# Optimization experiments

Measured on AMD Instinct MI355X. Metric: run time of the kernel, lower is better.

The kernel has to match this reference:

```python
import jax, jax.numpy as jnp
import numpy as np

N, E, D, H, ED = 10000, 160000, 512, 256, 16
EPS = 1e-5  # BatchNorm1d eps


def _cgconv(x, src, dst, edge_attr, Wf, bf, Ws, bs, gamma, beta, mean, var):
    # PyG CGConv: z = [x_i, x_j, e_ij]; m = sigmoid(lin_f(z)) * softplus(lin_s(z));
    # aggr='add' at target i; batch_norm (eval mode, running stats) then residual.
    z = jnp.concatenate([x[dst], x[src], edge_attr], axis=1)  # [E, 2D+ED]
    m = jax.nn.sigmoid(z @ Wf + bf) * jax.nn.softplus(z @ Ws + bs)  # [E, D]
    aggr = jax.ops.segment_sum(m, dst, num_segments=x.shape[0])  # [N, D]
    bn = (aggr - mean) * jax.lax.rsqrt(var + EPS) * gamma + beta
    return x + bn


def _gcnconv(x, src, dst, W, b):
    # PyG GCNConv with add_self_loops=True, normalize=True:
    n = x.shape[0]
    deg = jax.ops.segment_sum(jnp.ones((src.shape[0],), x.dtype), dst, num_segments=n) + 1.0
    dinv = jax.lax.rsqrt(deg)  # [N]
    h = x @ W  # [N, out]
    out = jax.ops.segment_sum((dinv[src] * dinv[dst])[:, None] * h[src], dst, num_segments=n)
    out = out + (dinv * dinv)[:, None] * h  # self-loop contribution
    return out + b


def _forward(x, edge_attr, goal_feat,
             cg1_Wf, cg1_bf, cg1_Ws, cg1_bs, cg1_gamma, cg1_beta, cg1_mean, cg1_var,
             cg2_Wf, cg2_bf, cg2_Ws, cg2_bs, cg2_gamma, cg2_beta, cg2_mean, cg2_var,
             gcn3_W, gcn3_b, gcn4_W, gcn4_b, d1_W, d1_b, d2_W, d2_b, src, dst):
    # dropout layers are identity in eval mode (self.training=False)
    x = jax.nn.relu(_cgconv(x, src, dst, edge_attr, cg1_Wf, cg1_bf, cg1_Ws, cg1_bs,
                            cg1_gamma, cg1_beta, cg1_mean, cg1_var))
    x = jax.nn.relu(_cgconv(x, src, dst, edge_attr, cg2_Wf, cg2_bf, cg2_Ws, cg2_bs,
                            cg2_gamma, cg2_beta, cg2_mean, cg2_var))
    x = jax.nn.relu(_gcnconv(x, src, dst, gcn3_W, gcn3_b))
    x = jax.nn.relu(_gcnconv(x, src, dst, gcn4_W, gcn4_b))
    g = jnp.broadcast_to(goal_feat, (x.shape[0], goal_feat.shape[1]))  # repeat(num_nodes, 1)
    h = jax.nn.relu(jnp.concatenate([x, g], axis=1) @ d1_W + d1_b)
    return h @ d2_W + d2_b  # [N, 1]


def setup_inputs() -> dict:
    ks = jax.random.split(jax.random.key(0), 12)
    w = lambda k, s: jax.random.normal(k, s, dtype=jnp.float32) * 0.02
    Z = 2 * D + ED
    return {
        "x": jax.random.normal(ks[0], (N, D), jnp.float32),
        "edge_attr": jax.random.normal(ks[1], (E, ED), jnp.float32),
        "goal_feat": jax.random.normal(ks[2], (1, D), jnp.float32),
        "cg1_Wf": w(ks[3], (Z, D)), "cg1_bf": jnp.zeros((D,), jnp.float32),
        "cg1_Ws": w(ks[4], (Z, D)), "cg1_bs": jnp.zeros((D,), jnp.float32),
        "cg1_gamma": jnp.ones((D,), jnp.float32), "cg1_beta": jnp.zeros((D,), jnp.float32),
        "cg1_mean": jnp.zeros((D,), jnp.float32), "cg1_var": jnp.ones((D,), jnp.float32),
        "cg2_Wf": w(ks[5], (Z, D)), "cg2_bf": jnp.zeros((D,), jnp.float32),
        "cg2_Ws": w(ks[6], (Z, D)), "cg2_bs": jnp.zeros((D,), jnp.float32),
        "cg2_gamma": jnp.ones((D,), jnp.float32), "cg2_beta": jnp.zeros((D,), jnp.float32),
        "cg2_mean": jnp.zeros((D,), jnp.float32), "cg2_var": jnp.ones((D,), jnp.float32),
        "gcn3_W": w(ks[7], (D, H)), "gcn3_b": jnp.zeros((H,), jnp.float32),
        "gcn4_W": w(ks[8], (H, H)), "gcn4_b": jnp.zeros((H,), jnp.float32),
        "d1_W": w(ks[9], (H + D, D)), "d1_b": jnp.zeros((D,), jnp.float32),
        "d2_W": w(ks[10], (D, 1)), "d2_b": jnp.zeros((1,), jnp.float32),
        "edge_index": jax.random.randint(ks[11], (2, E), 0, N, dtype=jnp.int32),
        "batch": jnp.zeros((N,), jnp.int32),
    }


def reference(x, edge_attr, goal_feat,
              cg1_Wf, cg1_bf, cg1_Ws, cg1_bs, cg1_gamma, cg1_beta, cg1_mean, cg1_var,
              cg2_Wf, cg2_bf, cg2_Ws, cg2_bs, cg2_gamma, cg2_beta, cg2_mean, cg2_var,
              gcn3_W, gcn3_b, gcn4_W, gcn4_b, d1_W, d1_b, d2_W, d2_b,
              edge_index, batch):
    src, dst = edge_index[0], edge_index[1]
    return _forward(x, edge_attr, goal_feat,
                    cg1_Wf, cg1_bf, cg1_Ws, cg1_bs, cg1_gamma, cg1_beta, cg1_mean, cg1_var,
                    cg2_Wf, cg2_bf, cg2_Ws, cg2_bs, cg2_gamma, cg2_beta, cg2_mean, cg2_var,
                    gcn3_W, gcn3_b, gcn4_W, gcn4_b, d1_W, d1_b, d2_W, d2_b, src, dst)
```

## Files before the change

### kernel.cpp

```cpp
#include <hip/hip_runtime.h>
#include <math.h>

#define N_NODES 10000
#define N_EDGES 160000
#define DIM 512
#define HDIM 256
#define EDIM 16
#define BN_EPS 1e-5f
#define L2E 1.4426950408889634f
#define LN2 0.6931471805599453f

typedef unsigned short ushort_t;
typedef unsigned int uint_t;
typedef __attribute__((ext_vector_type(8))) short bf16x8;
typedef __attribute__((ext_vector_type(4))) float f32x4;
typedef __attribute__((ext_vector_type(2))) _Float16 half2_t;

__device__ __forceinline__ ushort_t f2bf(float x) {
    uint_t u = __float_as_uint(x);
    uint_t r = (u + 0x7FFF + ((u >> 16) & 1)) >> 16;
    return (ushort_t)r;
}
__device__ __forceinline__ float bf2f(ushort_t h) {
    return __uint_as_float(((uint_t)h) << 16);
}
__device__ __forceinline__ float bflo(uint_t u) {
    return __uint_as_float(u << 16);
}
__device__ __forceinline__ float bfhi(uint_t u) {
    return __uint_as_float(u & 0xffff0000u);
}
__device__ __forceinline__ uint_t pk_bf(float a, float b) {
    return (uint_t)f2bf(a) | ((uint_t)f2bf(b) << 16);
}
__device__ __forceinline__ half2_t u2h(uint_t u) {
    return __builtin_bit_cast(half2_t, u);
}
__device__ __forceinline__ uint_t pk_f16(float a, float b) {
    return __builtin_bit_cast(uint_t, __builtin_amdgcn_cvt_pkrtz(a, b));
}
__device__ __forceinline__ void gld16(const void* g, void* l) {
    __builtin_amdgcn_global_load_lds(
        (const __attribute__((address_space(1))) unsigned int*)g,
        (__attribute__((address_space(3))) unsigned int*)l, 16, 0, 0);
}
__device__ __forceinline__ float fexp2(float x) {
#if __has_builtin(__builtin_amdgcn_exp2f)
    return __builtin_amdgcn_exp2f(x);
#else
    return __expf(x * LN2);
#endif
}
__device__ __forceinline__ float flog2(float x) {
#if __has_builtin(__builtin_amdgcn_logf)
    return __builtin_amdgcn_logf(x);
#else
    return __logf(x) * L2E;
#endif
}
__device__ __forceinline__ void swz(int lid, int gx, int gy, int& bx, int& by) {
    int per = gy * 8;
    int grp = lid / per;
    int rem = lid - grp * per;
    int gsz = min(8, gx - grp * 8);
    by = rem / gsz;
    bx = grp * 8 + (rem - by * gsz);
}

__global__ void k_hist(const int* __restrict__ dst, int* __restrict__ cnt) {
    int e = blockIdx.x * blockDim.x + threadIdx.x;
    if (e < N_EDGES) atomicAdd(&cnt[dst[e]], 1);
}

__global__ __launch_bounds__(1024) void k_scan(int* __restrict__ offs, float* __restrict__ dinv) {
    __shared__ int wsum[16];
    __shared__ int carryS;
    int t = threadIdx.x, lane = t & 63, wv = t >> 6;
    if (t == 0) carryS = 0;
    __syncthreads();
    for (int base = 0; base < N_NODES; base += 1024) {
        int idx = base + t;
        int v = (idx < N_NODES) ? offs[idx] : 0;
        if (idx < N_NODES) dinv[idx] = rsqrtf((float)v + 1.0f);
        int s = v;
#pragma unroll
        for (int off = 1; off < 64; off <<= 1) {
            int u = __shfl_up(s, off, 64);
            if (lane >= off) s += u;
        }
        if (lane == 63) wsum[wv] = s;
        __syncthreads();
        int carry = carryS;
        if (wv == 0) {
            int w = (lane < 16) ? wsum[lane] : 0;
#pragma unroll
            for (int off = 1; off < 16; off <<= 1) {
                int u = __shfl_up(w, off, 64);
                if (lane >= off) w += u;
            }
            if (lane < 16) wsum[lane] = w;
        }
        __syncthreads();
        int wbase = (wv == 0) ? 0 : wsum[wv - 1];
        if (idx < N_NODES) offs[idx] = carry + wbase + s - v;
        int total = wsum[15];
        __syncthreads();
        if (t == 0) carryS = carry + total;
        __syncthreads();
    }
    if (t == 0) offs[N_NODES] = carryS;
}

__global__ void k_scatter(const int* __restrict__ srcv, const int* __restrict__ dstv,
                          const float* __restrict__ ea,
                          const int* __restrict__ offs, const float* __restrict__ dinv,
                          int* __restrict__ cursor,
                          int* __restrict__ srcArr, float* __restrict__ dinvArr,
                          uint_t* __restrict__ eaP) {
    int e = blockIdx.x * blockDim.x + threadIdx.x;
    if (e >= N_EDGES) return;
    int d = dstv[e];
    int p = offs[d] + atomicAdd(&cursor[d], 1);
    int s = srcv[e];
    srcArr[p] = s;
    dinvArr[p] = dinv[s];
    const float* er = ea + (size_t)e * EDIM;
    uint_t pk[8];
#pragma unroll
    for (int k2 = 0; k2 < 8; k2++) pk[k2] = pk_f16(er[2 * k2], er[2 * k2 + 1]);
    uint_t* q = eaP + (size_t)p * 8;
    *(uint4*)q = *(uint4*)&pk[0];
    *(uint4*)(q + 4) = *(uint4*)&pk[4];
}

__global__ __launch_bounds__(256) void k_cvtW(
    const float* __restrict__ Wf0, const float* __restrict__ Ws0,
    const float* __restrict__ Wf1, const float* __restrict__ Ws1,
    const float* __restrict__ g3W, const float* __restrict__ g4W,
    const float* __restrict__ d1W,
    ushort_t* __restrict__ W2cg0, ushort_t* __restrict__ W2cg1,
    ushort_t* __restrict__ W2g3, ushort_t* __restrict__ W2g4,
    ushort_t* __restrict__ W2d1,
    int* __restrict__ offsZ, int* __restrict__ curZ, float* __restrict__ outZ)
{
    __shared__ ushort_t tle[64][72];
    int b = blockIdx.x, t = threadIdx.x;
    if (b >= 592) {
        int idx = (b - 592) * 256 + t;
        if (idx < 10001) offsZ[idx] = 0;
        else if (idx < 20001) curZ[idx - 10001] = 0;
        else if (idx < 30001) outZ[idx - 20001] = 0.f;
        return;
    }
    const float* src; int ldw, kin0, cin0, ldk, cout0, kout0; ushort_t* out; float scale;
    if (b < 512) {
        int layer = b >> 8, tt = b & 255;
        int g = tt >> 6, rem = tt & 63;
        int ct = rem >> 3, kt = rem & 7;
        const float* Wf = layer ? Wf1 : Wf0;
        const float* Ws = layer ? Ws1 : Ws0;
        src = (g & 1) ? Ws : Wf;
        ldw = 512; kin0 = ((g & 2) ? 512 : 0) + kt * 64; cin0 = ct * 64;
        out = layer ? W2cg1 : W2cg0; ldk = 512;
        cout0 = g * 512 + ct * 64; kout0 = kt * 64;
        scale = L2E;
    } else if (b < 544) {
        int tt = b - 512; int ct = tt >> 3, kt = tt & 7;
        src = g3W; ldw = 256; kin0 = kt * 64; cin0 = ct * 64;
        out = W2g3; ldk = 512; cout0 = ct * 64; kout0 = kt * 64; scale = 1.f;
    } else if (b < 560) {
        int tt = b - 544; int ct = tt >> 2, kt = tt & 3;
        src = g4W; ldw = 256; kin0 = kt * 64; cin0 = ct * 64;
        out = W2g4; ldk = 256; cout0 = ct * 64; kout0 = kt * 64; scale = 1.f;
    } else {
        int tt = b - 560; int ct = tt >> 2, kt = tt & 3;
        src = d1W; ldw = 512; kin0 = kt * 64; cin0 = ct * 64;
        out = W2d1; ldk = 256; cout0 = ct * 64; kout0 = kt * 64; scale = 1.f;
    }
    int c = t & 63;
    int k4 = t >> 6;
#pragma unroll
    for (int i = 0; i < 16; i++) {
        int k = k4 * 16 + i;
        tle[k][c] = f2bf(src[(size_t)(kin0 + k) * ldw + cin0 + c] * scale);
    }
    __syncthreads();
    int cl = t >> 2, kq = t & 3;
    ushort_t tmp[16];
#pragma unroll
    for (int j = 0; j < 16; j++) tmp[j] = tle[kq * 16 + j][cl];
    ushort_t* dst = out + (size_t)(cout0 + cl) * ldk + kout0 + kq * 16;
    *(uint4*)dst = *(uint4*)&tmp[0];
    *(uint4*)(dst + 8) = *(uint4*)&tmp[8];
}

#define MP_WEP   32
#define MP_GV    40
#define MP_END   20040

__global__ __launch_bounds__(256) void k_megaprep(
    const float* __restrict__ x, const float* __restrict__ goal,
    const float* __restrict__ Wf0, const float* __restrict__ Ws0,
    const float* __restrict__ Wf1, const float* __restrict__ Ws1,
    const float* __restrict__ d1W, const float* __restrict__ d1b,
    ushort_t* __restrict__ A2, uint_t* __restrict__ WEP, float* __restrict__ cgv)
{
    int b = blockIdx.x, t = threadIdx.x;
    if (b < MP_WEP) {
        int layer = b >> 4, blk = b & 15;
        int idx = blk * 256 + t;
        int c = idx >> 3, k2 = idx & 7;
        const float* Wf = (layer ? Wf1 : Wf0) + 1024 * 512;
        const float* Ws = (layer ? Ws1 : Ws0) + 1024 * 512;
        uint_t* WEPf = WEP + layer * 8192;
        uint_t* WEPs = WEPf + 4096;
        WEPf[c * 8 + k2] = pk_f16(Wf[(2 * k2) * 512 + c] * L2E, Wf[(2 * k2 + 1) * 512 + c] * L2E);
        WEPs[c * 8 + k2] = pk_f16(Ws[(2 * k2) * 512 + c] * L2E, Ws[(2 * k2 + 1) * 512 + c] * L2E);
    } else if (b < MP_GV) {
        __shared__ float red[256];
        int bb = b - MP_WEP;
        int c = bb * 64 + (t & 63);
        int slice = t >> 6;
        float acc = 0.f;
        for (int i = 0; i < 128; i++) {
            int k = slice * 128 + i;
            acc += goal[k] * d1W[(size_t)(256 + k) * 512 + c];
        }
        red[t] = acc;
        __syncthreads();
        if (t < 128) red[t] += red[t + 128];
        __syncthreads();
        if (t < 64) cgv[c] = red[t] + red[t + 64] + d1b[c];
    } else {
        int idx = (b - MP_GV) * 256 + t;
        if (idx < N_NODES * 512) A2[idx] = f2bf(x[idx]);
    }
}

__global__ __launch_bounds__(256) void k_gemm3(
    const ushort_t* __restrict__ A2, int K, int M,
    const ushort_t* __restrict__ W2t,
    float* __restrict__ outF, ushort_t* __restrict__ outQ,
    const float* __restrict__ bias, int mode, int ldc, int gx, int gy)
{
    __shared__ ushort_t As[128 * 64];
    __shared__ ushort_t Bs[128 * 64];
    int tid = threadIdx.x;
    int lane = tid & 63, w = tid >> 6;
    int wm = w & 1, wn = w >> 1;
    int lrow = lane & 15, quad = lane >> 4;
    int bx, by;
    swz(blockIdx.x, gx, gy, bx, by);
    int row0 = bx * 128, col0 = by * 128;

    f32x4 acc[4][4] = {};

    const ushort_t* ArG[4]; ushort_t* ArL[4];
    const ushort_t* BrG[4]; ushort_t* BrL[4];
#pragma unroll
    for (int p = 0; p < 4; p++) {
        int s = tid + 256 * p;
        int r = s >> 3, k8p = s & 7;
        int k8l = k8p ^ (r & 7);
        int gra = row0 + r; if (gra >= M) gra = M - 1;
        ArG[p] = A2 + (size_t)gra * K + k8l * 8;
        ArL[p] = As + s * 8;
        BrG[p] = W2t + (size_t)(col0 + r) * K + k8l * 8;
        BrL[p] = Bs + s * 8;
    }
    const ushort_t* afp[2][4];
    const ushort_t* bfp[2][4];
#pragma unroll
    for (int sl = 0; sl < 2; sl++)
#pragma unroll
        for (int mt = 0; mt < 4; mt++) {
            int r = wm * 64 + mt * 16 + lrow;
            afp[sl][mt] = As + (r * 8 + ((sl * 4 + quad) ^ (r & 7))) * 8;
            int c = wn * 64 + mt * 16 + lrow;
            bfp[sl][mt] = Bs + (c * 8 + ((sl * 4 + quad) ^ (c & 7))) * 8;
        }

    for (int k0 = 0; k0 < K; k0 += 64) {
        __syncthreads();
#pragma unroll
        for (int p = 0; p < 4; p++) {
            gld16(ArG[p] + k0, ArL[p]);
            gld16(BrG[p] + k0, BrL[p]);
        }
        __syncthreads();
#pragma unroll
        for (int sl = 0; sl < 2; sl++) {
            bf16x8 af[4], bff[4];
#pragma unroll
            for (int i = 0; i < 4; i++) {
                af[i]  = *(const bf16x8*)afp[sl][i];
                bff[i] = *(const bf16x8*)bfp[sl][i];
            }
#pragma unroll
            for (int mt = 0; mt < 4; mt++)
#pragma unroll
                for (int nt = 0; nt < 4; nt++)
                    acc[mt][nt] = __builtin_amdgcn_mfma_f32_16x16x32_bf16(
                        af[mt], bff[nt], acc[mt][nt], 0, 0, 0);
        }
    }

#pragma unroll
    for (int mt = 0; mt < 4; mt++) {
#pragma unroll
        for (int nt = 0; nt < 4; nt++) {
            int gcol = col0 + wn * 64 + nt * 16 + lrow;
#pragma unroll
            for (int r = 0; r < 4; r++) {
                int grow = row0 + wm * 64 + mt * 16 + quad * 4 + r;
                if (grow >= M) continue;
                float v = acc[mt][nt][r];
                if (mode == 1) {
                    if (gcol < 1024) {
                        outF[(size_t)grow * 1024 + gcol] = v;
                    } else {
                        int c = gcol - 1024;
                        int grp = c >> 9, cc = c & 511;
                        int pos = (cc >> 1) * 4 + grp * 2 + (cc & 1);
                        outQ[(size_t)grow * 1024 + pos] = f2bf(v);
                    }
                } else if (mode == 2) {
                    outF[(size_t)grow * ldc + gcol] = fmaxf(v + bias[gcol], 0.f);
                } else {
                    outQ[(size_t)grow * ldc + gcol] = f2bf(v);
                }
            }
        }
    }
}

__global__ __launch_bounds__(256) void k_gemm64(
    const ushort_t* __restrict__ A2, int K, int M,
    const ushort_t* __restrict__ W2t,
    float* __restrict__ outF, ushort_t* __restrict__ outQ,
    const float* __restrict__ bias, int mode, int ldc, int gx, int gy,
    const float* __restrict__ d2w, const float* __restrict__ d2b,
    float* __restrict__ outG)
{
    __shared__ ushort_t As[64 * 64];
    __shared__ ushort_t Bs[128 * 64];
    __shared__ float part[64];
    int tid = threadIdx.x;
    int lane = tid & 63, w = tid >> 6;
    int lrow = lane & 15, quad = lane >> 4;
    int bx, by;
    swz(blockIdx.x, gx, gy, bx, by);
    int row0 = bx * 64, col0 = by * 128;

    f32x4 acc[4][2] = {};

    const ushort_t* ArG[2]; ushort_t* ArL[2];
    const ushort_t* BrG[4]; ushort_t* BrL[4];
#pragma unroll
    for (int p = 0; p < 2; p++) {
        int s = tid + 256 * p;
        int r = s >> 3, k8p = s & 7;
        int k8l = k8p ^ (r & 7);
        int gra = row0 + r; if (gra >= M) gra = M - 1;
        ArG[p] = A2 + (size_t)gra * K + k8l * 8;
        ArL[p] = As + s * 8;
    }
#pragma unroll
    for (int p = 0; p < 4; p++) {
        int s = tid + 256 * p;
        int r = s >> 3, k8p = s & 7;
        int k8l = k8p ^ (r & 7);
        BrG[p] = W2t + (size_t)(col0 + r) * K + k8l * 8;
        BrL[p] = Bs + s * 8;
    }
    const ushort_t* afp[2][4];
    const ushort_t* bfp[2][2];
#pragma unroll
    for (int sl = 0; sl < 2; sl++) {
#pragma unroll
        for (int mt = 0; mt < 4; mt++) {
            int r = mt * 16 + lrow;
            afp[sl][mt] = As + (r * 8 + ((sl * 4 + quad) ^ (r & 7))) * 8;
        }
#pragma unroll
        for (int nt = 0; nt < 2; nt++) {
            int c = w * 32 + nt * 16 + lrow;
            bfp[sl][nt] = Bs + (c * 8 + ((sl * 4 + quad) ^ (c & 7))) * 8;
        }
    }

    if (mode == 4 && tid < 64) part[tid] = 0.f;

    for (int k0 = 0; k0 < K; k0 += 64) {
        __syncthreads();
        gld16(ArG[0] + k0, ArL[0]);
        gld16(ArG[1] + k0, ArL[1]);
#pragma unroll
        for (int p = 0; p < 4; p++) gld16(BrG[p] + k0, BrL[p]);
        __syncthreads();
#pragma unroll
        for (int sl = 0; sl < 2; sl++) {
            bf16x8 af[4], bff[2];
#pragma unroll
            for (int i = 0; i < 4; i++) af[i] = *(const bf16x8*)afp[sl][i];
#pragma unroll
            for (int i = 0; i < 2; i++) bff[i] = *(const bf16x8*)bfp[sl][i];
#pragma unroll
            for (int mt = 0; mt < 4; mt++)
#pragma unroll
                for (int nt = 0; nt < 2; nt++)
                    acc[mt][nt] = __builtin_amdgcn_mfma_f32_16x16x32_bf16(
                        af[mt], bff[nt], acc[mt][nt], 0, 0, 0);
        }
    }

    if (mode == 4) {
        float w2c[2], bc[2];
#pragma unroll
        for (int nt = 0; nt < 2; nt++) {
            int gcol = col0 + w * 32 + nt * 16 + lrow;
            w2c[nt] = d2w[gcol];
            bc[nt] = bias[gcol];
        }
        __syncthreads();
#pragma unroll
        for (int mt = 0; mt < 4; mt++) {
#pragma unroll
            for (int r = 0; r < 4; r++) {
                float rp = 0.f;
#pragma unroll
                for (int nt = 0; nt < 2; nt++) {
                    float v = fmaxf(acc[mt][nt][r] + bc[nt], 0.f);
                    rp = fmaf(v, w2c[nt], rp);
                }
                atomicAdd(&part[mt * 16 + quad * 4 + r], rp);
            }
        }
        __syncthreads();
        if (tid < 64) {
            int grow = row0 + tid;
            if (grow < M) {
                float v = part[tid];
                if (by == 0) v += d2b[0];
                atomicAdd(&outG[grow], v);
            }
        }
        return;
    }

#pragma unroll
    for (int mt = 0; mt < 4; mt++) {
#pragma unroll
        for (int nt = 0; nt < 2; nt++) {
            int gcol = col0 + w * 32 + nt * 16 + lrow;
#pragma unroll
            for (int r = 0; r < 4; r++) {
                int grow = row0 + mt * 16 + quad * 4 + r;
                if (grow >= M) continue;
                float v = acc[mt][nt][r];
                if (mode == 2) outF[(size_t)grow * ldc + gcol] = fmaxf(v + bias[gcol], 0.f);
                else outQ[(size_t)grow * ldc + gcol] = f2bf(v);
            }
        }
    }
}

__global__ __launch_bounds__(256) void k_cg_aggr(
    const float* __restrict__ xin, const float* __restrict__ P,
    const ushort_t* __restrict__ Qi,
    const uint_t* __restrict__ WEPf, const uint_t* __restrict__ WEPs,
    const float* __restrict__ bfv, const float* __restrict__ bsv,
    const float* __restrict__ gamma, const float* __restrict__ beta,
    const float* __restrict__ mean, const float* __restrict__ var,
    const int* __restrict__ offs, const int* __restrict__ srcArr,
    const uint_t* __restrict__ eaP,
    float* __restrict__ xout, ushort_t* __restrict__ A2out)
{
    int i = blockIdx.x;
    int t = threadIdx.x;
    int c0 = 2 * t;
    uint_t wfp[2][8], wsp[2][8];
    {
        const uint_t* pf8 = WEPf + c0 * 8;
        const uint_t* ps8 = WEPs + c0 * 8;
        *(uint4*)&wfp[0][0] = *(const uint4*)(pf8 + 0);
        *(uint4*)&wfp[0][4] = *(const uint4*)(pf8 + 4);
        *(uint4*)&wfp[1][0] = *(const uint4*)(pf8 + 8);
        *(uint4*)&wfp[1][4] = *(const uint4*)(pf8 + 12);
        *(uint4*)&wsp[0][0] = *(const uint4*)(ps8 + 0);
        *(uint4*)&wsp[0][4] = *(const uint4*)(ps8 + 4);
        *(uint4*)&wsp[1][0] = *(const uint4*)(ps8 + 8);
        *(uint4*)&wsp[1][4] = *(const uint4*)(ps8 + 12);
    }
    float2 pf = *(const float2*)&P[(size_t)i * 1024 + c0];
    float2 ps = *(const float2*)&P[(size_t)i * 1024 + 512 + c0];
    float2 bf2 = *(const float2*)&bfv[c0];
    float2 bs2 = *(const float2*)&bsv[c0];
    pf.x = fmaf(bf2.x, L2E, pf.x); pf.y = fmaf(bf2.y, L2E, pf.y);
    ps.x = fmaf(bs2.x, L2E, ps.x); ps.y = fmaf(bs2.y, L2E, ps.y);
    float acc0 = 0.f, acc1 = 0.f;
    int e0 = offs[i], e1 = offs[i + 1];
    __shared__ uint_t sEaP[32][8];
    __shared__ int sSrc[34];
    const ushort_t* Qbase = Qi + 4 * t;
    for (int base = e0; base < e1; base += 32) {
        int g = min(32, e1 - base);
        __syncthreads();
        if (t < 34) {
            int s = 0;
            if (t < g) s = srcArr[base + t];
            sSrc[t] = s;
        }
        {
            int j = t >> 3, k2 = t & 7;
            if (j < g) sEaP[j][k2] = eaP[(size_t)(base + j) * 8 + k2];
        }
        __syncthreads();
        uint2 q0 = *(const uint2*)(Qbase + ((size_t)sSrc[0] << 10));
        uint2 q1 = *(const uint2*)(Qbase + ((size_t)sSrc[1] << 10));
        for (int j = 0; j < g; j++) {
            uint2 qn = *(const uint2*)(Qbase + ((size_t)sSrc[j + 2] << 10));
            uint4 eA = *(const uint4*)&sEaP[j][0];
            uint4 eB = *(const uint4*)&sEaP[j][4];
            float gf0 = pf.x + bflo(q0.x), gf1 = pf.y + bfhi(q0.x);
            float gs0 = ps.x + bflo(q0.y), gs1 = ps.y + bfhi(q0.y);
            uint_t ek[8] = {eA.x, eA.y, eA.z, eA.w, eB.x, eB.y, eB.z, eB.w};
#pragma unroll
            for (int k = 0; k < 8; k++) {
                half2_t e2 = u2h(ek[k]);
                gf0 = __builtin_amdgcn_fdot2(e2, u2h(wfp[0][k]), gf0, false);
                gf1 = __builtin_amdgcn_fdot2(e2, u2h(wfp[1][k]), gf1, false);
                gs0 = __builtin_amdgcn_fdot2(e2, u2h(wsp[0][k]), gs0, false);
                gs1 = __builtin_amdgcn_fdot2(e2, u2h(wsp[1][k]), gs1, false);
            }
            float sg0 = __builtin_amdgcn_rcpf(1.f + fexp2(-gf0));
            float sg1 = __builtin_amdgcn_rcpf(1.f + fexp2(-gf1));
            float sp0 = fmaxf(gs0, 0.f) + flog2(1.f + fexp2(-fabsf(gs0)));
            float sp1 = fmaxf(gs1, 0.f) + flog2(1.f + fexp2(-fabsf(gs1)));
            acc0 = fmaf(sg0, sp0, acc0);
            acc1 = fmaf(sg1, sp1, acc1);
            q0 = q1; q1 = qn;
        }
    }
    acc0 *= LN2;
    acc1 *= LN2;
    size_t ib = (size_t)i * DIM;
    float2 mn = *(const float2*)&mean[c0];
    float2 vr = *(const float2*)&var[c0];
    float2 gm = *(const float2*)&gamma[c0];
    float2 bt = *(const float2*)&beta[c0];
    float2 xi = *(const float2*)&xin[ib + c0];
    float bn0 = (acc0 - mn.x) * rsqrtf(vr.x + BN_EPS) * gm.x + bt.x;
    float bn1 = (acc1 - mn.y) * rsqrtf(vr.y + BN_EPS) * gm.y + bt.y;
    float o0 = fmaxf(xi.x + bn0, 0.f);
    float o1 = fmaxf(xi.y + bn1, 0.f);
    if (xout) *(float2*)&xout[ib + c0] = make_float2(o0, o1);
    *(uint_t*)(A2out + (size_t)i * 512 + c0) = pk_bf(o0, o1);
}

__global__ __launch_bounds__(128) void k_gcn_aggr(
    const ushort_t* __restrict__ h, const float* __restrict__ dinv,
    const float* __restrict__ bias,
    const int* __restrict__ offs, const int* __restrict__ srcArr,
    const float* __restrict__ dinvArr, ushort_t* __restrict__ A2out)
{
    int i = blockIdx.x;
    int t = threadIdx.x;
    int c0 = 2 * t;
    float acc0 = 0.f, acc1 = 0.f;
    int e0 = offs[i], e1 = offs[i + 1];
    __shared__ int sS[36];
    __shared__ float sD[36];
    for (int base = e0; base < e1; base += 32) {
        int g = min(32, e1 - base);
        __syncthreads();
        if (t < 36) {
            bool ok = (t < g);
            sS[t] = ok ? srcArr[base + t] : 0;
            sD[t] = ok ? dinvArr[base + t] : 0.f;
        }
        __syncthreads();
        uint_t q0 = *(const uint_t*)(h + (size_t)sS[0] * HDIM + c0);
        uint_t q1 = *(const uint_t*)(h + (size_t)sS[1] * HDIM + c0);
        uint_t q2 = *(const uint_t*)(h + (size_t)sS[2] * HDIM + c0);
        uint_t q3 = *(const uint_t*)(h + (size_t)sS[3] * HDIM + c0);
        for (int j = 0; j < g; j++) {
            uint_t qn = *(const uint_t*)(h + (size_t)sS[j + 4] * HDIM + c0);
            acc0 += sD[j] * bflo(q0);
            acc1 += sD[j] * bfhi(q0);
            q0 = q1; q1 = q2; q2 = q3; q3 = qn;
        }
    }
    float di = dinv[i];
    uint_t qi = *(const uint_t*)(h + (size_t)i * HDIM + c0);
    float2 b2 = *(const float2*)&bias[c0];
    float o0 = fmaxf(di * acc0 + di * di * bflo(qi) + b2.x, 0.f);
    float o1 = fmaxf(di * acc1 + di * di * bfhi(qi) + b2.y, 0.f);
    *(uint_t*)(A2out + (size_t)i * 256 + c0) = pk_bf(o0, o1);
}

extern "C" void kernel_launch(void* const* d_in, const int* in_sizes, int n_in,
                              void* d_out, int out_size, void* d_ws, size_t ws_size,
                              hipStream_t stream) {
    (void)in_sizes; (void)n_in; (void)out_size; (void)ws_size;
    const float* x      = (const float*)d_in[0];
    const float* ea     = (const float*)d_in[1];
    const float* goal   = (const float*)d_in[2];
    const float* cgWf[2] = {(const float*)d_in[3],  (const float*)d_in[11]};
    const float* cgbf[2] = {(const float*)d_in[4],  (const float*)d_in[12]};
    const float* cgWs[2] = {(const float*)d_in[5],  (const float*)d_in[13]};
    const float* cgbs[2] = {(const float*)d_in[6],  (const float*)d_in[14]};
    const float* cggm[2] = {(const float*)d_in[7],  (const float*)d_in[15]};
    const float* cgbt[2] = {(const float*)d_in[8],  (const float*)d_in[16]};
    const float* cgmn[2] = {(const float*)d_in[9],  (const float*)d_in[17]};
    const float* cgvr[2] = {(const float*)d_in[10], (const float*)d_in[18]};
    const float* gcn3_W = (const float*)d_in[19];
    const float* gcn3_b = (const float*)d_in[20];
    const float* gcn4_W = (const float*)d_in[21];
    const float* gcn4_b = (const float*)d_in[22];
    const float* d1_W   = (const float*)d_in[23];
    const float* d1_b   = (const float*)d_in[24];
    const float* d2_W   = (const float*)d_in[25];
    const float* d2_b   = (const float*)d_in[26];
    const int*   eidx   = (const int*)d_in[27];
    const int*   srcv   = eidx;
    const int*   dstv   = eidx + N_EDGES;
    float* outp = (float*)d_out;

    char* w = (char*)d_ws;
    float*    Pbuf  = (float*)w;                      w += (size_t)N_NODES * 1024 * 4;
    ushort_t* Qbuf  = (ushort_t*)w;                   w += (size_t)N_NODES * 1024 * 2;
    float*    xB    = (float*)w;                      w += (size_t)N_NODES * 512 * 4;
    ushort_t* A2    = (ushort_t*)w;                   w += (size_t)N_NODES * 512 * 2;
    ushort_t* A3    = (ushort_t*)w;                   w += (size_t)N_NODES * 256 * 2;
    ushort_t* W2cg0 = (ushort_t*)w;                   w += (size_t)2048 * 512 * 2;
    ushort_t* W2cg1 = (ushort_t*)w;                   w += (size_t)2048 * 512 * 2;
    ushort_t* W2g3  = (ushort_t*)w;                   w += (size_t)256 * 512 * 2;
    ushort_t* W2g4  = (ushort_t*)w;                   w += (size_t)256 * 256 * 2;
    ushort_t* W2d1  = (ushort_t*)w;                   w += (size_t)512 * 256 * 2;
    uint_t*   eaP   = (uint_t*)w;                     w += (size_t)N_EDGES * 8 * 4;
    uint_t*   WEP   = (uint_t*)w;                     w += 16384 * 4;
    float*    cgv   = (float*)w;                      w += 512 * 4;
    int*      srcArr  = (int*)w;                      w += N_EDGES * 4;
    float*    dinvArr = (float*)w;                    w += N_EDGES * 4;
    int*      offs    = (int*)w;                      w += (N_NODES + 1) * 4;
    int*      cursor  = (int*)w;                      w += N_NODES * 4;
    float*    dinv    = (float*)w;                    w += N_NODES * 4;
    uint_t* WEPf[2] = {WEP, WEP + 8192};
    uint_t* WEPs[2] = {WEP + 4096, WEP + 12288};
    ushort_t* h3 = (ushort_t*)Pbuf;

    k_cvtW<<<710, 256, 0, stream>>>(cgWf[0], cgWs[0], cgWf[1], cgWs[1],
                                    gcn3_W, gcn4_W, d1_W,
                                    W2cg0, W2cg1, W2g3, W2g4, W2d1,
                                    offs, cursor, outp);
    k_megaprep<<<MP_END, 256, 0, stream>>>(x, goal,
        cgWf[0], cgWs[0], cgWf[1], cgWs[1], d1_W, d1_b, A2, WEP, cgv);

    k_hist<<<(N_EDGES + 255) / 256, 256, 0, stream>>>(dstv, offs);
    k_scan<<<1, 1024, 0, stream>>>(offs, dinv);
    k_scatter<<<(N_EDGES + 255) / 256, 256, 0, stream>>>(srcv, dstv, ea, offs, dinv,
                                                         cursor, srcArr, dinvArr, eaP);

    k_gemm3<<<79 * 16, 256, 0, stream>>>(A2, 512, N_NODES, W2cg0,
                                         Pbuf, Qbuf, nullptr, 1, 0, 79, 16);
    k_cg_aggr<<<N_NODES, 256, 0, stream>>>(x, Pbuf, Qbuf, WEPf[0], WEPs[0],
                                           cgbf[0], cgbs[0],
                                           cggm[0], cgbt[0], cgmn[0], cgvr[0],
                                           offs, srcArr, eaP, xB, A2);
    k_gemm3<<<79 * 16, 256, 0, stream>>>(A2, 512, N_NODES, W2cg1,
                                         Pbuf, Qbuf, nullptr, 1, 0, 79, 16);
    k_cg_aggr<<<N_NODES, 256, 0, stream>>>(xB, Pbuf, Qbuf, WEPf[1], WEPs[1],
                                           cgbf[1], cgbs[1],
                                           cggm[1], cgbt[1], cgmn[1], cgvr[1],
                                           offs, srcArr, eaP, nullptr, A2);

    k_gemm64<<<157 * 2, 256, 0, stream>>>(A2, 512, N_NODES, W2g3,
                                          nullptr, h3, nullptr, 3, HDIM, 157, 2,
                                          nullptr, nullptr, nullptr);
    k_gcn_aggr<<<N_NODES, 128, 0, stream>>>(h3, dinv, gcn3_b, offs, srcArr, dinvArr, A3);

    k_gemm64<<<157 * 2, 256, 0, stream>>>(A3, 256, N_NODES, W2g4,
                                          nullptr, h3, nullptr, 3, HDIM, 157, 2,
                                          nullptr, nullptr, nullptr);
    k_gcn_aggr<<<N_NODES, 128, 0, stream>>>(h3, dinv, gcn4_b, offs, srcArr, dinvArr, A3);

    k_gemm64<<<157 * 4, 256, 0, stream>>>(A3, 256, N_NODES, W2d1,
                                          nullptr, nullptr, cgv, 4, DIM, 157, 4,
                                          d2_W, d2_b, outp);
}
```

Baseline: 563.1 us.

## Compute edge-attribute projection with bf16 MFMA per 8-edge chunk in CG aggregation

Replaces the per-thread fp16 dot2 loop that projected the 16-dim edge attributes onto each channel with a per-chunk bf16 MFMA. It computes the projections for 8 edges across all 512 channels into shared memory, and the per-edge loop then reads them back. Edge attributes and edge weights are now packed as bf16 rather than fp16, which lowers precision. Chunks shrink from 32 to 8 edges, so there are more barriers, half of each 16-row MFMA is wasted, and the weights are reloaded from global memory for every chunk.

```diff
diff --git a/kernel.cpp b/kernel.cpp
--- a/kernel.cpp
+++ b/kernel.cpp
@@ -14,7 +14,6 @@
 typedef unsigned int uint_t;
 typedef __attribute__((ext_vector_type(8))) short bf16x8;
 typedef __attribute__((ext_vector_type(4))) float f32x4;
-typedef __attribute__((ext_vector_type(2))) _Float16 half2_t;
 
 __device__ __forceinline__ ushort_t f2bf(float x) {
     uint_t u = __float_as_uint(x);
@@ -32,12 +31,6 @@
 }
 __device__ __forceinline__ uint_t pk_bf(float a, float b) {
     return (uint_t)f2bf(a) | ((uint_t)f2bf(b) << 16);
-}
-__device__ __forceinline__ half2_t u2h(uint_t u) {
-    return __builtin_bit_cast(half2_t, u);
-}
-__device__ __forceinline__ uint_t pk_f16(float a, float b) {
-    return __builtin_bit_cast(uint_t, __builtin_amdgcn_cvt_pkrtz(a, b));
 }
 __device__ __forceinline__ void gld16(const void* g, void* l) {
     __builtin_amdgcn_global_load_lds(
@@ -127,7 +120,7 @@
     const float* er = ea + (size_t)e * EDIM;
     uint_t pk[8];
 #pragma unroll
-    for (int k2 = 0; k2 < 8; k2++) pk[k2] = pk_f16(er[2 * k2], er[2 * k2 + 1]);
+    for (int k2 = 0; k2 < 8; k2++) pk[k2] = pk_bf(er[2 * k2], er[2 * k2 + 1]);
     uint_t* q = eaP + (size_t)p * 8;
     *(uint4*)q = *(uint4*)&pk[0];
     *(uint4*)(q + 4) = *(uint4*)&pk[4];
@@ -214,8 +207,8 @@
         const float* Ws = (layer ? Ws1 : Ws0) + 1024 * 512;
         uint_t* WEPf = WEP + layer * 8192;
         uint_t* WEPs = WEPf + 4096;
-        WEPf[c * 8 + k2] = pk_f16(Wf[(2 * k2) * 512 + c] * L2E, Wf[(2 * k2 + 1) * 512 + c] * L2E);
-        WEPs[c * 8 + k2] = pk_f16(Ws[(2 * k2) * 512 + c] * L2E, Ws[(2 * k2 + 1) * 512 + c] * L2E);
+        WEPf[c * 8 + k2] = pk_bf(Wf[(2 * k2) * 512 + c] * L2E, Wf[(2 * k2 + 1) * 512 + c] * L2E);
+        WEPs[c * 8 + k2] = pk_bf(Ws[(2 * k2) * 512 + c] * L2E, Ws[(2 * k2 + 1) * 512 + c] * L2E);
     } else if (b < MP_GV) {
         __shared__ float red[256];
         int bb = b - MP_WEP;
@@ -478,20 +471,12 @@
 {
     int i = blockIdx.x;
     int t = threadIdx.x;
+    int w = t >> 6, lane = t & 63;
+    int lrow = lane & 15, quad = lane >> 4;
     int c0 = 2 * t;
-    uint_t wfp[2][8], wsp[2][8];
-    {
-        const uint_t* pf8 = WEPf + c0 * 8;
-        const uint_t* ps8 = WEPs + c0 * 8;
-        *(uint4*)&wfp[0][0] = *(const uint4*)(pf8 + 0);
-        *(uint4*)&wfp[0][4] = *(const uint4*)(pf8 + 4);
-        *(uint4*)&wfp[1][0] = *(const uint4*)(pf8 + 8);
-        *(uint4*)&wfp[1][4] = *(const uint4*)(pf8 + 12);
-        *(uint4*)&wsp[0][0] = *(const uint4*)(ps8 + 0);
-        *(uint4*)&wsp[0][4] = *(const uint4*)(ps8 + 4);
-        *(uint4*)&wsp[1][0] = *(const uint4*)(ps8 + 8);
-        *(uint4*)&wsp[1][4] = *(const uint4*)(ps8 + 12);
-    }
+    __shared__ uint_t sEaP[8][8];
+    __shared__ int sSrc[10];
+    __shared__ uint_t sFS[8][516];
     float2 pf = *(const float2*)&P[(size_t)i * 1024 + c0];
     float2 ps = *(const float2*)&P[(size_t)i * 1024 + 512 + c0];
     float2 bf2 = *(const float2*)&bfv[c0];
@@ -500,39 +485,55 @@
     ps.x = fmaf(bs2.x, L2E, ps.x); ps.y = fmaf(bs2.y, L2E, ps.y);
     float acc0 = 0.f, acc1 = 0.f;
     int e0 = offs[i], e1 = offs[i + 1];
-    __shared__ uint_t sEaP[32][8];
-    __shared__ int sSrc[34];
     const ushort_t* Qbase = Qi + 4 * t;
-    for (int base = e0; base < e1; base += 32) {
-        int g = min(32, e1 - base);
-        __syncthreads();
-        if (t < 34) {
-            int s = 0;
-            if (t < g) s = srcArr[base + t];
-            sSrc[t] = s;
-        }
+    for (int base = e0; base < e1; base += 8) {
+        int g = min(8, e1 - base);
+        __syncthreads();
+        if (t < 10) {
+            sSrc[t] = (t < g) ? srcArr[base + t] : 0;
+        } else if (t >= 64 && t < 128) {
+            int tt = t - 64;
+            int j = tt >> 3, k2 = tt & 7;
+            sEaP[j][k2] = (j < g) ? eaP[(size_t)(base + j) * 8 + k2] : 0u;
+        }
+        __syncthreads();
+        bf16x8 eb;
         {
-            int j = t >> 3, k2 = t & 7;
-            if (j < g) sEaP[j][k2] = eaP[(size_t)(base + j) * 8 + k2];
-        }
-        __syncthreads();
+            uint4 u = make_uint4(0, 0, 0, 0);
+            if (lrow < 8 && quad < 2) u = *(const uint4*)&sEaP[lrow][(quad & 1) * 4];
+            eb = __builtin_bit_cast(bf16x8, u);
+        }
+#pragma unroll
+        for (int nt = 0; nt < 8; nt++) {
+            int chA = w * 128 + nt * 16 + lrow;
+            uint4 uf = make_uint4(0, 0, 0, 0), us4 = make_uint4(0, 0, 0, 0);
+            if (quad < 2) {
+                uf  = *(const uint4*)&WEPf[chA * 8 + (quad & 1) * 4];
+                us4 = *(const uint4*)&WEPs[chA * 8 + (quad & 1) * 4];
+            }
+            f32x4 cf = {0.f, 0.f, 0.f, 0.f};
+            f32x4 cs = {0.f, 0.f, 0.f, 0.f};
+            cf = __builtin_amdgcn_mfma_f32_16x16x32_bf16(
+                __builtin_bit_cast(bf16x8, uf), eb, cf, 0, 0, 0);
+            cs = __builtin_amdgcn_mfma_f32_16x16x32_bf16(
+                __builtin_bit_cast(bf16x8, us4), eb, cs, 0, 0, 0);
+            if (lrow < 8) {
+                int chW = w * 128 + nt * 16 + quad * 4;
+                uint_t o[4];
+#pragma unroll
+                for (int r = 0; r < 4; r++) o[r] = pk_bf(cf[r], cs[r]);
+                *(uint4*)&sFS[lrow][chW] = *(uint4*)&o[0];
+            }
+        }
         uint2 q0 = *(const uint2*)(Qbase + ((size_t)sSrc[0] << 10));
         uint2 q1 = *(const uint2*)(Qbase + ((size_t)sSrc[1] << 10));
         for (int j = 0; j < g; j++) {
             uint2 qn = *(const uint2*)(Qbase + ((size_t)sSrc[j + 2] << 10));
-            uint4 eA = *(const uint4*)&sEaP[j][0];
-            uint4 eB = *(const uint4*)&sEaP[j][4];
-            float gf0 = pf.x + bflo(q0.x), gf1 = pf.y + bfhi(q0.x);
-            float gs0 = ps.x + bflo(q0.y), gs1 = ps.y + bfhi(q0.y);
-            uint_t ek[8] = {eA.x, eA.y, eA.z, eA.w, eB.x, eB.y, eB.z, eB.w};
-#pragma unroll
-            for (int k = 0; k < 8; k++) {
-                half2_t e2 = u2h(ek[k]);
-                gf0 = __builtin_amdgcn_fdot2(e2, u2h(wfp[0][k]), gf0, false);
-                gf1 = __builtin_amdgcn_fdot2(e2, u2h(wfp[1][k]), gf1, false);
-                gs0 = __builtin_amdgcn_fdot2(e2, u2h(wsp[0][k]), gs0, false);
-                gs1 = __builtin_amdgcn_fdot2(e2, u2h(wsp[1][k]), gs1, false);
-            }
+            uint2 fs = *(const uint2*)&sFS[j][c0];
+            float gf0 = pf.x + bflo(q0.x) + bflo(fs.x);
+            float gf1 = pf.y + bfhi(q0.x) + bflo(fs.y);
+            float gs0 = ps.x + bflo(q0.y) + bfhi(fs.x);
+            float gs1 = ps.y + bfhi(q0.y) + bfhi(fs.y);
             float sg0 = __builtin_amdgcn_rcpf(1.f + fexp2(-gf0));
             float sg1 = __builtin_amdgcn_rcpf(1.f + fexp2(-gf1));
             float sp0 = fmaxf(gs0, 0.f) + flog2(1.f + fexp2(-fabsf(gs0)));
```

New measurement: 629.7 us. +11.8%, slower.
